# Performance work log

Measured on AMD Instinct MI355X. Metric: run time of the kernel, lower is better.

## Reference

```python
import jax, jax.numpy as jnp
import numpy as np

DIM = 1024
N_HEADS = 16
HEAD_DIM = DIM // N_HEADS
FF_DIM = 4096
EPS = 1e-8


def rms_norm(x, scale):
    # norm = ||x||_2 * d^{-1/2}; out = scale * x / (norm + eps)
    norm = jnp.linalg.norm(x, axis=-1, keepdims=True) * (x.shape[-1] ** -0.5)
    return scale * x / (norm + EPS)


def rope_cos_sin(seq_len, dtype=jnp.float32):
    # inv_freq over even indices of head_dim; after the truncation branch in
    # apply_rotary_pos_emb, effective cos/sin have size head_dim//2.
    inv_freq = 1.0 / (10000.0 ** (jnp.arange(0, HEAD_DIM, 2, dtype=jnp.float32) / HEAD_DIM))
    t = jnp.arange(seq_len, dtype=jnp.float32)
    freqs = t[:, None] * inv_freq[None, :]  # [S, head_dim//2]
    return jnp.cos(freqs).astype(dtype), jnp.sin(freqs).astype(dtype)


def apply_rope(x, cos, sin):
    # x: [B, S, H, hd]; cos/sin: [S, hd//2] broadcast over batch and heads
    c = cos[None, :, None, :]
    s = sin[None, :, None, :]
    x1, x2 = jnp.split(x, 2, axis=-1)
    return jnp.concatenate([x1 * c - x2 * s, x1 * s + x2 * c], axis=-1)


def setup_inputs() -> dict:
    key = jax.random.key(0)
    ks = jax.random.split(key, 10)
    B, S = 2, 2048
    std = DIM ** -0.5
    inp = {
        "x": jax.random.normal(ks[0], (B, S, DIM), jnp.float32),
        "mask": jnp.tril(jnp.ones((S, S), dtype=bool)),
        "qkv_w": jax.random.normal(ks[1], (3 * DIM, DIM), jnp.float32) * std,
        "attn_out_w": jax.random.normal(ks[2], (DIM, DIM), jnp.float32) * std,
        "gate_w": jax.random.normal(ks[3], (FF_DIM, DIM), jnp.float32) * std,
        "gate_b": jnp.zeros((FF_DIM,), jnp.float32),
        "lin_w": jax.random.normal(ks[4], (FF_DIM, DIM), jnp.float32) * std,
        "lin_b": jnp.zeros((FF_DIM,), jnp.float32),
        "ff_out_w": jax.random.normal(ks[5], (DIM, FF_DIM), jnp.float32) * (FF_DIM ** -0.5),
        "norm1_scale": jnp.ones((DIM,), jnp.float32),
        "norm2_scale": jnp.ones((DIM,), jnp.float32),
    }
    return inp


def reference(x, mask, qkv_w, attn_out_w, gate_w, gate_b, lin_w, lin_b,
              ff_out_w, norm1_scale, norm2_scale):
    B, S, _ = x.shape
    residual = x
    qkv = (x @ qkv_w.T).reshape(B, S, 3, N_HEADS, HEAD_DIM)
    q, k, v = qkv[:, :, 0], qkv[:, :, 1], qkv[:, :, 2]  # [B,S,H,hd]
    cos, sin = rope_cos_sin(S, x.dtype)
    q = apply_rope(q, cos, sin)
    k = apply_rope(k, cos, sin)
    # naive full attention, materializing [B,H,S,S] as the source does
    scores = jnp.einsum('bqhd,bkhd->bhqk', q, k) / jnp.sqrt(jnp.asarray(HEAD_DIM, x.dtype))
    scores = jnp.where(mask[None, None, :, :], scores, jnp.asarray(-1e9, x.dtype))
    attn = jax.nn.softmax(scores, axis=-1)
    out = jnp.einsum('bhqk,bkhd->bqhd', attn, v).reshape(B, S, DIM)
    out = out @ attn_out_w.T
    x = rms_norm(residual + out, norm1_scale)
    residual = x
    ff = jax.nn.sigmoid(x @ gate_w.T + gate_b) * (x @ lin_w.T + lin_b)
    ff = ff @ ff_out_w.T
    x = rms_norm(residual + ff, norm2_scale)
    return x
```

## Files before the change

kernel.cpp:

```cpp
#include <hip/hip_runtime.h>
#include <hip/hip_bf16.h>
#include <math.h>

#define DIMSZ 1024
#define NHEAD 16
#define HDIM 64
#define FFDIM 4096
#define SEQ 2048
#define NBATCH 2

typedef unsigned short ushortt;
typedef __attribute__((ext_vector_type(8))) short frag8;
typedef __attribute__((ext_vector_type(4))) float f32x4;

__device__ __forceinline__ float u2f(ushortt u) {
  return __uint_as_float(((unsigned)u) << 16);
}
__device__ __forceinline__ ushortt f2bu(float f) {
  unsigned x = __float_as_uint(f);
  return (ushortt)((x + 0x7FFFu + ((x >> 16) & 1u)) >> 16);
}

__global__ __launch_bounds__(256) void cast_f2b(
    const float* __restrict__ src, ushortt* __restrict__ dst, int n) {
  int i = (blockIdx.x * 256 + threadIdx.x) * 4;
  if (i >= n) return;
  float4 f = *(const float4*)(src + i);
  ushort4 u;
  u.x = f2bu(f.x); u.y = f2bu(f.y); u.z = f2bu(f.z); u.w = f2bu(f.w);
  *(ushort4*)(dst + i) = u;
}

__global__ __launch_bounds__(256) void cast_ff_chunk(
    const float* __restrict__ gate_w, const float* __restrict__ lin_w,
    const float* __restrict__ ffout_w, int c,
    ushortt* __restrict__ gcb, ushortt* __restrict__ lcb,
    ushortt* __restrict__ focb) {
  const int M1 = 1048576;
  int t = (blockIdx.x * 256 + threadIdx.x) * 4;
  const float* src;
  ushortt* dst;
  int e;
  if (t < M1) {
    e = t; src = gate_w + (size_t)c * M1 + e; dst = gcb + e;
  } else if (t < 2 * M1) {
    e = t - M1; src = lin_w + (size_t)c * M1 + e; dst = lcb + e;
  } else {
    e = t - 2 * M1;
    int n = e >> 10, k = e & 1023;
    src = ffout_w + (size_t)n * FFDIM + c * 1024 + k; dst = focb + e;
  }
  float4 f = *(const float4*)src;
  ushort4 u;
  u.x = f2bu(f.x); u.y = f2bu(f.y); u.z = f2bu(f.z); u.w = f2bu(f.w);
  *(ushort4*)dst = u;
}

template <int EPI>
__global__ __launch_bounds__(256) void gemm_mfma(
    const ushortt* __restrict__ A, const ushortt* __restrict__ W,
    void* __restrict__ Cv, const float* __restrict__ bias,
    const ushortt* __restrict__ other, int M, int N, int K, int first) {
  __shared__ __align__(16) short As[2][128 * 32];
  __shared__ __align__(16) short Bs[2][128 * 32];
  const int tid = threadIdx.x;
  const int wave = tid >> 6;
  const int lane = tid & 63;
  const int bm = blockIdx.y * 128;
  const int bn = blockIdx.x * 128;
  const int wm = (wave >> 1) * 64;
  const int wn = (wave & 1) * 64;

  f32x4 acc[4][4] = {};

  const int sr = lane >> 2;
  const int sc = (lane & 3) * 8;
  const ushortt* pa0 = A + (size_t)(bm + wave * 16 + sr) * K + sc;
  const ushortt* pa1 = pa0 + (size_t)64 * K;
  const ushortt* pb0 = W + (size_t)(bn + wave * 16 + sr) * K + sc;
  const ushortt* pb1 = pb0 + (size_t)64 * K;
  const int lo0 = (wave * 16) * 32;
  const int lo1 = (64 + wave * 16) * 32;

  const int fr = lane & 15;
  const int fq = (lane >> 4) * 8;
  const int nt = K >> 5;

  auto stage = [&](int t, int buf) {
    const int ko = t * 32;
    short* ab = &As[0][0] + buf * 4096;
    short* bb = &Bs[0][0] + buf * 4096;
    __builtin_amdgcn_global_load_lds(
        (const __attribute__((address_space(1))) void*)(pa0 + ko),
        (__attribute__((address_space(3))) void*)(ab + lo0), 16, 0, 0);
    __builtin_amdgcn_global_load_lds(
        (const __attribute__((address_space(1))) void*)(pa1 + ko),
        (__attribute__((address_space(3))) void*)(ab + lo1), 16, 0, 0);
    __builtin_amdgcn_global_load_lds(
        (const __attribute__((address_space(1))) void*)(pb0 + ko),
        (__attribute__((address_space(3))) void*)(bb + lo0), 16, 0, 0);
    __builtin_amdgcn_global_load_lds(
        (const __attribute__((address_space(1))) void*)(pb1 + ko),
        (__attribute__((address_space(3))) void*)(bb + lo1), 16, 0, 0);
  };

  stage(0, 0);
  __syncthreads();

  for (int t = 0; t < nt; ++t) {
    if (t + 1 < nt) stage(t + 1, (t + 1) & 1);
    const short* as = &As[0][0] + (t & 1) * 4096;
    const short* bs = &Bs[0][0] + (t & 1) * 4096;

    frag8 af[4], bf[4];
#pragma unroll
    for (int mi = 0; mi < 4; ++mi)
      af[mi] = *(const frag8*)&as[(wm + mi * 16 + fr) * 32 + fq];
#pragma unroll
    for (int ni = 0; ni < 4; ++ni)
      bf[ni] = *(const frag8*)&bs[(wn + ni * 16 + fr) * 32 + fq];
#pragma unroll
    for (int mi = 0; mi < 4; ++mi)
#pragma unroll
      for (int ni = 0; ni < 4; ++ni)
        acc[mi][ni] = __builtin_amdgcn_mfma_f32_16x16x32_bf16(
            af[mi], bf[ni], acc[mi][ni], 0, 0, 0);
    __syncthreads();
  }

  const int er = (lane >> 4) * 4;
  const int ec = lane & 15;
#pragma unroll
  for (int mi = 0; mi < 4; ++mi)
#pragma unroll
    for (int ni = 0; ni < 4; ++ni)
#pragma unroll
      for (int r = 0; r < 4; ++r) {
        int m = bm + wm + mi * 16 + er + r;
        int n = bn + wn + ni * 16 + ec;
        size_t o = (size_t)m * N + n;
        float v = acc[mi][ni][r];
        if (EPI == 0) {
          ((float*)Cv)[o] = v;
        } else if (EPI == 1) {
          ((ushortt*)Cv)[o] = f2bu(v);
        } else {
          float* C = (float*)Cv;
          C[o] = first ? v : C[o] + v;
        }
      }
}

__global__ __launch_bounds__(256) void gemm_gatelin(
    const ushortt* __restrict__ A, const ushortt* __restrict__ Wg,
    const ushortt* __restrict__ Wl, ushortt* __restrict__ Cv,
    const float* __restrict__ gbias, const float* __restrict__ lbias,
    int M, int N, int K) {
  __shared__ __align__(16) short As[2][128 * 32];
  __shared__ __align__(16) short Gs[2][128 * 32];
  __shared__ __align__(16) short Ls[2][128 * 32];
  const int tid = threadIdx.x;
  const int wave = tid >> 6;
  const int lane = tid & 63;
  const int bm = blockIdx.y * 128;
  const int bn = blockIdx.x * 128;
  const int wm = (wave >> 1) * 64;
  const int wn = (wave & 1) * 64;

  f32x4 accg[4][4] = {};
  f32x4 accl[4][4] = {};

  const int sr = lane >> 2;
  const int sc = (lane & 3) * 8;
  const ushortt* pa0 = A + (size_t)(bm + wave * 16 + sr) * K + sc;
  const ushortt* pa1 = pa0 + (size_t)64 * K;
  const ushortt* pg0 = Wg + (size_t)(bn + wave * 16 + sr) * K + sc;
  const ushortt* pg1 = pg0 + (size_t)64 * K;
  const ushortt* pl0 = Wl + (size_t)(bn + wave * 16 + sr) * K + sc;
  const ushortt* pl1 = pl0 + (size_t)64 * K;
  const int lo0 = (wave * 16) * 32;
  const int lo1 = (64 + wave * 16) * 32;

  const int fr = lane & 15;
  const int fq = (lane >> 4) * 8;
  const int nt = K >> 5;

  auto stage = [&](int t, int buf) {
    const int ko = t * 32;
    short* ab = &As[0][0] + buf * 4096;
    short* gb = &Gs[0][0] + buf * 4096;
    short* lb = &Ls[0][0] + buf * 4096;
    __builtin_amdgcn_global_load_lds(
        (const __attribute__((address_space(1))) void*)(pa0 + ko),
        (__attribute__((address_space(3))) void*)(ab + lo0), 16, 0, 0);
    __builtin_amdgcn_global_load_lds(
        (const __attribute__((address_space(1))) void*)(pa1 + ko),
        (__attribute__((address_space(3))) void*)(ab + lo1), 16, 0, 0);
    __builtin_amdgcn_global_load_lds(
        (const __attribute__((address_space(1))) void*)(pg0 + ko),
        (__attribute__((address_space(3))) void*)(gb + lo0), 16, 0, 0);
    __builtin_amdgcn_global_load_lds(
        (const __attribute__((address_space(1))) void*)(pg1 + ko),
        (__attribute__((address_space(3))) void*)(gb + lo1), 16, 0, 0);
    __builtin_amdgcn_global_load_lds(
        (const __attribute__((address_space(1))) void*)(pl0 + ko),
        (__attribute__((address_space(3))) void*)(lb + lo0), 16, 0, 0);
    __builtin_amdgcn_global_load_lds(
        (const __attribute__((address_space(1))) void*)(pl1 + ko),
        (__attribute__((address_space(3))) void*)(lb + lo1), 16, 0, 0);
  };

  stage(0, 0);
  __syncthreads();

  for (int t = 0; t < nt; ++t) {
    if (t + 1 < nt) stage(t + 1, (t + 1) & 1);
    const short* as = &As[0][0] + (t & 1) * 4096;
    const short* gs = &Gs[0][0] + (t & 1) * 4096;
    const short* ls = &Ls[0][0] + (t & 1) * 4096;

    frag8 af[4], gf[4], lf[4];
#pragma unroll
    for (int mi = 0; mi < 4; ++mi)
      af[mi] = *(const frag8*)&as[(wm + mi * 16 + fr) * 32 + fq];
#pragma unroll
    for (int ni = 0; ni < 4; ++ni) {
      gf[ni] = *(const frag8*)&gs[(wn + ni * 16 + fr) * 32 + fq];
      lf[ni] = *(const frag8*)&ls[(wn + ni * 16 + fr) * 32 + fq];
    }
#pragma unroll
    for (int mi = 0; mi < 4; ++mi)
#pragma unroll
      for (int ni = 0; ni < 4; ++ni) {
        accg[mi][ni] = __builtin_amdgcn_mfma_f32_16x16x32_bf16(
            af[mi], gf[ni], accg[mi][ni], 0, 0, 0);
        accl[mi][ni] = __builtin_amdgcn_mfma_f32_16x16x32_bf16(
            af[mi], lf[ni], accl[mi][ni], 0, 0, 0);
      }
    __syncthreads();
  }

  const int er = (lane >> 4) * 4;
  const int ec = lane & 15;
#pragma unroll
  for (int mi = 0; mi < 4; ++mi)
#pragma unroll
    for (int ni = 0; ni < 4; ++ni)
#pragma unroll
      for (int r = 0; r < 4; ++r) {
        int m = bm + wm + mi * 16 + er + r;
        int n = bn + wn + ni * 16 + ec;
        size_t o = (size_t)m * N + n;
        float g = accg[mi][ni][r] + gbias[n];
        float l = accl[mi][ni][r] + lbias[n];
        float sig = 1.0f / (1.0f + __expf(-g));
        ((ushortt*)Cv)[o] = f2bu(sig * l);
      }
}

__global__ __launch_bounds__(256) void rope_prep(
    const ushortt* __restrict__ qkv, ushortt* __restrict__ Qr,
    ushortt* __restrict__ Kr, ushortt* __restrict__ Vr) {
  const int s0 = blockIdx.x * 64;
  const int bh = blockIdx.y;
  const int b = bh >> 4, h = bh & 15;
  const int tid = threadIdx.x;
  __shared__ float ifr_s[32];
  __shared__ ushortt vt[64][72];
  if (tid < 32) ifr_s[tid] = __powf(10000.0f, -(float)tid * (1.0f / 32.0f));
  __syncthreads();
  const size_t qbase = (size_t)bh * SEQ * 64;

#pragma unroll
  for (int i = 0; i < 8; ++i) {
    int p = i * 256 + tid;
    int r = p >> 5, d = p & 31;
    size_t src = ((size_t)(b * SEQ + s0 + r)) * (3 * DIMSZ) + h * 64 + d;
    float q1 = u2f(qkv[src]), q2 = u2f(qkv[src + 32]);
    float k1 = u2f(qkv[src + DIMSZ]), k2 = u2f(qkv[src + DIMSZ + 32]);
    float ang = (float)(s0 + r) * ifr_s[d];
    float sn, cs;
    __sincosf(ang, &sn, &cs);
    size_t dst = qbase + (size_t)(s0 + r) * 64 + d;
    Qr[dst]      = f2bu((q1 * cs - q2 * sn) * 0.125f);
    Qr[dst + 32] = f2bu((q1 * sn + q2 * cs) * 0.125f);
    Kr[dst]      = f2bu(k1 * cs - k2 * sn);
    Kr[dst + 32] = f2bu(k1 * sn + k2 * cs);
  }

#pragma unroll
  for (int i = 0; i < 2; ++i) {
    int e = (i * 256 + tid) * 8;
    int r = e >> 6, d0 = e & 63;
    size_t src = ((size_t)(b * SEQ + s0 + r)) * (3 * DIMSZ) + 2 * DIMSZ + h * 64 + d0;
    *(ushort4*)&vt[r][d0]     = *(const ushort4*)(qkv + src);
    *(ushort4*)&vt[r][d0 + 4] = *(const ushort4*)(qkv + src + 4);
  }
  __syncthreads();
  {
    int d = tid >> 2;
    int sc0 = (tid & 3) * 16;
    size_t dst = (size_t)bh * 64 * SEQ + (size_t)blockIdx.x * 4096 +
                 (size_t)d * 64 + sc0;
    ushortt tmp[16];
#pragma unroll
    for (int j = 0; j < 16; ++j) tmp[j] = vt[sc0 + j][d];
    *(ushort4*)(Vr + dst)      = *(ushort4*)&tmp[0];
    *(ushort4*)(Vr + dst + 4)  = *(ushort4*)&tmp[4];
    *(ushort4*)(Vr + dst + 8)  = *(ushort4*)&tmp[8];
    *(ushort4*)(Vr + dst + 12) = *(ushort4*)&tmp[12];
  }
}

__global__ __launch_bounds__(512) void flash_mfma(
    const ushortt* __restrict__ Qr, const ushortt* __restrict__ Kr,
    const ushortt* __restrict__ Vr, ushortt* __restrict__ ctx) {
  const int id = blockIdx.x;
  const int qt = id >> 5;
  const int bh = id & 31;
  const int q0 = qt * 128;
  const int b = bh >> 4, h = bh & 15;
  const int tid = threadIdx.x;
  const int w = tid >> 6;
  const int lane = tid & 63;
  const int fr = lane & 15;
  const int quad = lane >> 4;

  __shared__ __align__(16) short Kb[2][4096];
  __shared__ __align__(16) short Vb[2][4096];
  __shared__ __align__(16) ushortt Ps[8][16][72];

  const size_t qkbase = (size_t)bh * SEQ * 64;
  const size_t vbase = (size_t)bh * 64 * SEQ;

  const int lin = (w << 10) + ((lane & 63) << 4);
  const int swz = lin ^ (((lin >> 7) & 7) << 4);
  const char* ksrc = (const char*)(Kr + qkbase) + swz;
  const char* vsrc = (const char*)(Vr + vbase) + swz;
  short* kdst[2] = {&Kb[0][w * 512], &Kb[1][w * 512]};
  short* vdst[2] = {&Vb[0][w * 512], &Vb[1][w * 512]};

  frag8 aq[2];
#pragma unroll
  for (int hh = 0; hh < 2; ++hh)
    aq[hh] = *(const frag8*)(Qr + qkbase + (size_t)(q0 + w * 16 + fr) * 64 +
                             hh * 32 + quad * 8);

  float mr[4], lr[4];
  f32x4 od[4] = {};
#pragma unroll
  for (int r = 0; r < 4; ++r) { mr[r] = -1e30f; lr[r] = 0.0f; }

  const int nt = 2 * qt + 2;

  __builtin_amdgcn_global_load_lds(
      (const __attribute__((address_space(1))) void*)ksrc,
      (__attribute__((address_space(3))) void*)kdst[0], 16, 0, 0);
  __builtin_amdgcn_global_load_lds(
      (const __attribute__((address_space(1))) void*)vsrc,
      (__attribute__((address_space(3))) void*)vdst[0], 16, 0, 0);
  __syncthreads();

  for (int t = 0; t < nt; ++t) {
    const int c0 = t * 64;
    if (t + 1 < nt) {
      const char* kn = ksrc + (size_t)(t + 1) * 8192;
      const char* vn = vsrc + (size_t)(t + 1) * 8192;
      __builtin_amdgcn_global_load_lds(
          (const __attribute__((address_space(1))) void*)kn,
          (__attribute__((address_space(3))) void*)kdst[(t + 1) & 1], 16, 0, 0);
      __builtin_amdgcn_global_load_lds(
          (const __attribute__((address_space(1))) void*)vn,
          (__attribute__((address_space(3))) void*)vdst[(t + 1) & 1], 16, 0, 0);
    }
    const char* kcur = (const char*)Kb[t & 1];
    const char* vcur = (const char*)Vb[t & 1];

    if (c0 <= q0 + w * 16 + 15) {
      f32x4 sc[4] = {};
#pragma unroll
      for (int ni = 0; ni < 4; ++ni)
#pragma unroll
        for (int hh = 0; hh < 2; ++hh) {
          int kb = (((ni * 16 + fr) << 7) + (hh << 6) + (quad << 4)) ^
                   ((fr & 7) << 4);
          frag8 kf = *(const frag8*)(kcur + kb);
          sc[ni] = __builtin_amdgcn_mfma_f32_16x16x32_bf16(aq[hh], kf, sc[ni],
                                                           0, 0, 0);
        }

      if (c0 + 63 > q0 + w * 16) {
        int rowb = q0 + w * 16 + quad * 4;
#pragma unroll
        for (int ni = 0; ni < 4; ++ni) {
          int col = c0 + ni * 16 + fr;
#pragma unroll
          for (int r = 0; r < 4; ++r)
            if (col > rowb + r) sc[ni][r] = -1e30f;
        }
      }

#pragma unroll
      for (int r = 0; r < 4; ++r) {
        float cm = fmaxf(fmaxf(sc[0][r], sc[1][r]), fmaxf(sc[2][r], sc[3][r]));
        for (int off = 1; off < 16; off <<= 1)
          cm = fmaxf(cm, __shfl_xor(cm, off, 16));
        float mn = fmaxf(mr[r], cm);
        float corr = __expf(mr[r] - mn);
        mr[r] = mn;
        float ps = 0.0f;
#pragma unroll
        for (int ni = 0; ni < 4; ++ni) {
          float p = __expf(sc[ni][r] - mn);
          Ps[w][quad * 4 + r][ni * 16 + fr] = f2bu(p);
          ps += p;
        }
        for (int off = 1; off < 16; off <<= 1) ps += __shfl_xor(ps, off, 16);
        lr[r] = lr[r] * corr + ps;
#pragma unroll
        for (int dt = 0; dt < 4; ++dt) od[dt][r] *= corr;
      }

      frag8 pf[2];
#pragma unroll
      for (int hh = 0; hh < 2; ++hh)
        pf[hh] = *(const frag8*)&Ps[w][fr][hh * 32 + quad * 8];
#pragma unroll
      for (int dt = 0; dt < 4; ++dt)
#pragma unroll
        for (int hh = 0; hh < 2; ++hh) {
          int vb_ = (((dt * 16 + fr) << 7) + (hh << 6) + (quad << 4)) ^
                    ((fr & 7) << 4);
          frag8 vf = *(const frag8*)(vcur + vb_);
          od[dt] = __builtin_amdgcn_mfma_f32_16x16x32_bf16(pf[hh], vf, od[dt],
                                                           0, 0, 0);
        }
    }
    __syncthreads();
  }

#pragma unroll
  for (int r = 0; r < 4; ++r) {
    float inv = 1.0f / lr[r];
    size_t row = (size_t)(b * SEQ + q0 + w * 16 + quad * 4 + r) * DIMSZ + h * 64;
#pragma unroll
    for (int dt = 0; dt < 4; ++dt)
      ctx[row + dt * 16 + fr] = f2bu(od[dt][r] * inv);
  }
}

template <int DUAL>
__global__ __launch_bounds__(256) void add_rmsnorm(
    const float* __restrict__ res, const float* __restrict__ proj,
    const float* __restrict__ scale, float* __restrict__ out,
    ushortt* __restrict__ out2) {
  const int row = blockIdx.x;
  const int tid = threadIdx.x;
  const size_t base = (size_t)row * DIMSZ;
  __shared__ float red[4];
  float y[4];
  float ss = 0.0f;
#pragma unroll
  for (int j = 0; j < 4; ++j) {
    int d = tid + j * 256;
    float yv = res[base + d] + proj[base + d];
    y[j] = yv;
    ss += yv * yv;
  }
  for (int off = 1; off < 64; off <<= 1) ss += __shfl_xor(ss, off, 64);
  if ((tid & 63) == 0) red[tid >> 6] = ss;
  __syncthreads();
  float tot = red[0] + red[1] + red[2] + red[3];
  float norm = sqrtf(tot) * 0.03125f;
  float inv = 1.0f / (norm + 1e-8f);
#pragma unroll
  for (int j = 0; j < 4; ++j) {
    int d = tid + j * 256;
    float v = scale[d] * y[j] * inv;
    out[base + d] = v;
    if (DUAL) out2[base + d] = f2bu(v);
  }
}

extern "C" void kernel_launch(void* const* d_in, const int* in_sizes, int n_in,
                              void* d_out, int out_size, void* d_ws, size_t ws_size,
                              hipStream_t stream) {
  const float* x          = (const float*)d_in[0];
  const float* qkv_w      = (const float*)d_in[2];
  const float* attn_out_w = (const float*)d_in[3];
  const float* gate_w     = (const float*)d_in[4];
  const float* gate_b     = (const float*)d_in[5];
  const float* lin_w      = (const float*)d_in[6];
  const float* lin_b      = (const float*)d_in[7];
  const float* ff_out_w   = (const float*)d_in[8];
  const float* n1s        = (const float*)d_in[9];
  const float* n2s        = (const float*)d_in[10];
  float* out = (float*)d_out;

  const int M = NBATCH * SEQ;
  char* ws = (char*)d_ws;
  char* dob = (char*)d_out;
  const size_t MB = 1 << 20;
  ushortt* qkv_tmp = (ushortt*)(ws + 0);
  ushortt* xb      = (ushortt*)(ws + 24 * MB);
  ushortt* qkv_wb  = (ushortt*)(ws + 32 * MB);
  ushortt* Qr      = (ushortt*)(ws + 24 * MB);
  ushortt* Kr      = (ushortt*)(ws + 32 * MB);
  ushortt* Vr      = (ushortt*)(ws + 40 * MB);
  ushortt* attn_wb = (ushortt*)(ws + 24 * MB);
  float*   proj    = (float*)(ws + 0);
  float*   x1      = (float*)(ws + 16 * MB);
  ushortt* x1b     = (ushortt*)(ws + 32 * MB);
  float*   proj2   = (float*)(ws + 0);
  ushortt* gcb     = (ushortt*)(ws + 40 * MB);
  ushortt* lcb     = (ushortt*)(ws + 42 * MB);
  ushortt* focb    = (ushortt*)(ws + 44 * MB);
  ushortt* ctx  = (ushortt*)(dob + 0);
  ushortt* ffc  = (ushortt*)(dob + 0);

  cast_f2b<<<4194304 / 1024, 256, 0, stream>>>(x, xb, 4194304);
  cast_f2b<<<3145728 / 1024, 256, 0, stream>>>(qkv_w, qkv_wb, 3145728);
  gemm_mfma<1><<<dim3(3072 / 128, M / 128), 256, 0, stream>>>(
      xb, qkv_wb, qkv_tmp, nullptr, nullptr, M, 3072, DIMSZ, 0);
  rope_prep<<<dim3(SEQ / 64, NBATCH * NHEAD), 256, 0, stream>>>(
      qkv_tmp, Qr, Kr, Vr);
  flash_mfma<<<(SEQ / 128) * NBATCH * NHEAD, 512, 0, stream>>>(
      Qr, Kr, Vr, ctx);
  cast_f2b<<<1048576 / 1024, 256, 0, stream>>>(attn_out_w, attn_wb, 1048576);
  gemm_mfma<0><<<dim3(DIMSZ / 128, M / 128), 256, 0, stream>>>(
      ctx, attn_wb, proj, nullptr, nullptr, M, DIMSZ, DIMSZ, 0);
  add_rmsnorm<1><<<M, 256, 0, stream>>>(x, proj, n1s, x1, x1b);
  for (int c = 0; c < 4; ++c) {
    cast_ff_chunk<<<3072, 256, 0, stream>>>(gate_w, lin_w, ff_out_w, c,
                                            gcb, lcb, focb);
    gemm_gatelin<<<dim3(1024 / 128, M / 128), 256, 0, stream>>>(
        x1b, gcb, lcb, ffc, gate_b + c * 1024, lin_b + c * 1024,
        M, 1024, DIMSZ);
    gemm_mfma<4><<<dim3(DIMSZ / 128, M / 128), 256, 0, stream>>>(
        ffc, focb, proj2, nullptr, nullptr, M, DIMSZ, 1024, c == 0 ? 1 : 0);
  }
  add_rmsnorm<0><<<M, 256, 0, stream>>>(x1, proj2, n2s, out, nullptr);
}
```

Measured before the change: 615.1 us.

## Fuse ff_out weight cast into GEMM, halve FF chunks, balance causal attention order

Adds a gemm_ffout kernel that loads fp32 ff_out weights directly, converts them to bf16 in registers and stages them through LDS, which removes the separate cast of that weight. The FF loop now runs 2 chunks of 2048 instead of 4 chunks of 1024, giving fewer launches and fewer read-modify-write passes over proj2. Flash attention block ids are remapped so the second half of the grid visits query tiles in reverse order, to balance the uneven causal work across the grid. The risk is extra per-thread conversion work and register pressure inside the ff_out GEMM mainloop.

```diff
diff --git a/kernel.cpp b/kernel.cpp
--- a/kernel.cpp
+++ b/kernel.cpp
@@ -31,36 +31,10 @@
   *(ushort4*)(dst + i) = u;
 }
 
-__global__ __launch_bounds__(256) void cast_ff_chunk(
-    const float* __restrict__ gate_w, const float* __restrict__ lin_w,
-    const float* __restrict__ ffout_w, int c,
-    ushortt* __restrict__ gcb, ushortt* __restrict__ lcb,
-    ushortt* __restrict__ focb) {
-  const int M1 = 1048576;
-  int t = (blockIdx.x * 256 + threadIdx.x) * 4;
-  const float* src;
-  ushortt* dst;
-  int e;
-  if (t < M1) {
-    e = t; src = gate_w + (size_t)c * M1 + e; dst = gcb + e;
-  } else if (t < 2 * M1) {
-    e = t - M1; src = lin_w + (size_t)c * M1 + e; dst = lcb + e;
-  } else {
-    e = t - 2 * M1;
-    int n = e >> 10, k = e & 1023;
-    src = ffout_w + (size_t)n * FFDIM + c * 1024 + k; dst = focb + e;
-  }
-  float4 f = *(const float4*)src;
-  ushort4 u;
-  u.x = f2bu(f.x); u.y = f2bu(f.y); u.z = f2bu(f.z); u.w = f2bu(f.w);
-  *(ushort4*)dst = u;
-}
-
 template <int EPI>
 __global__ __launch_bounds__(256) void gemm_mfma(
     const ushortt* __restrict__ A, const ushortt* __restrict__ W,
-    void* __restrict__ Cv, const float* __restrict__ bias,
-    const ushortt* __restrict__ other, int M, int N, int K, int first) {
+    void* __restrict__ Cv, int M, int N, int K) {
   __shared__ __align__(16) short As[2][128 * 32];
   __shared__ __align__(16) short Bs[2][128 * 32];
   const int tid = threadIdx.x;
@@ -142,11 +116,8 @@
         float v = acc[mi][ni][r];
         if (EPI == 0) {
           ((float*)Cv)[o] = v;
-        } else if (EPI == 1) {
+        } else {
           ((ushortt*)Cv)[o] = f2bu(v);
-        } else {
-          float* C = (float*)Cv;
-          C[o] = first ? v : C[o] + v;
         }
       }
 }
@@ -258,6 +229,113 @@
       }
 }
 
+__global__ __launch_bounds__(256) void gemm_ffout(
+    const ushortt* __restrict__ A, const float* __restrict__ Bw,
+    float* __restrict__ C, int lda, int koff, int first) {
+  __shared__ __align__(16) short As[2][128 * 32];
+  __shared__ __align__(16) short Bs[2][128 * 32];
+  const int tid = threadIdx.x;
+  const int wave = tid >> 6;
+  const int lane = tid & 63;
+  const int bm = blockIdx.y * 128;
+  const int bn = blockIdx.x * 128;
+  const int wm = (wave >> 1) * 64;
+  const int wn = (wave & 1) * 64;
+
+  f32x4 acc[4][4] = {};
+
+  const int sr = lane >> 2;
+  const int sc = (lane & 3) * 8;
+  const ushortt* pa0 = A + (size_t)(bm + wave * 16 + sr) * lda + sc;
+  const ushortt* pa1 = pa0 + (size_t)64 * lda;
+  const int lo0 = (wave * 16) * 32;
+  const int lo1 = (64 + wave * 16) * 32;
+
+  const int br = tid >> 2;
+  const int kc = (tid & 3) * 8;
+  const float* pb0 = Bw + (size_t)(bn + br) * FFDIM + koff + kc;
+  const float* pb1 = pb0 + (size_t)64 * FFDIM;
+
+  const int fr = lane & 15;
+  const int fq = (lane >> 4) * 8;
+  const int nt = 2048 >> 5;
+
+  float4 f0, f1, f2, f3;
+  auto bload = [&](int t) {
+    const float* p0 = pb0 + t * 32;
+    const float* p1 = pb1 + t * 32;
+    f0 = *(const float4*)p0; f1 = *(const float4*)(p0 + 4);
+    f2 = *(const float4*)p1; f3 = *(const float4*)(p1 + 4);
+  };
+  auto pk = [&](float4 a, float4 b) {
+    frag8 v;
+    v[0] = (short)f2bu(a.x); v[1] = (short)f2bu(a.y);
+    v[2] = (short)f2bu(a.z); v[3] = (short)f2bu(a.w);
+    v[4] = (short)f2bu(b.x); v[5] = (short)f2bu(b.y);
+    v[6] = (short)f2bu(b.z); v[7] = (short)f2bu(b.w);
+    return v;
+  };
+  auto bwrite = [&](int buf) {
+    *(frag8*)&Bs[buf][tid * 8] = pk(f0, f1);
+    *(frag8*)&Bs[buf][2048 + tid * 8] = pk(f2, f3);
+  };
+  auto astage = [&](int t, int buf) {
+    const int ko = t * 32;
+    short* ab = &As[0][0] + buf * 4096;
+    __builtin_amdgcn_global_load_lds(
+        (const __attribute__((address_space(1))) void*)(pa0 + ko),
+        (__attribute__((address_space(3))) void*)(ab + lo0), 16, 0, 0);
+    __builtin_amdgcn_global_load_lds(
+        (const __attribute__((address_space(1))) void*)(pa1 + ko),
+        (__attribute__((address_space(3))) void*)(ab + lo1), 16, 0, 0);
+  };
+
+  astage(0, 0);
+  bload(0);
+  bwrite(0);
+  __syncthreads();
+
+  for (int t = 0; t < nt; ++t) {
+    if (t + 1 < nt) {
+      astage(t + 1, (t + 1) & 1);
+      bload(t + 1);
+    }
+    const short* as = &As[0][0] + (t & 1) * 4096;
+    const short* bs = &Bs[0][0] + (t & 1) * 4096;
+
+    frag8 af[4], bf[4];
+#pragma unroll
+    for (int mi = 0; mi < 4; ++mi)
+      af[mi] = *(const frag8*)&as[(wm + mi * 16 + fr) * 32 + fq];
+#pragma unroll
+    for (int ni = 0; ni < 4; ++ni)
+      bf[ni] = *(const frag8*)&bs[(wn + ni * 16 + fr) * 32 + fq];
+#pragma unroll
+    for (int mi = 0; mi < 4; ++mi)
+#pragma unroll
+      for (int ni = 0; ni < 4; ++ni)
+        acc[mi][ni] = __builtin_amdgcn_mfma_f32_16x16x32_bf16(
+            af[mi], bf[ni], acc[mi][ni], 0, 0, 0);
+    if (t + 1 < nt) bwrite((t + 1) & 1);
+    __syncthreads();
+  }
+
+  const int er = (lane >> 4) * 4;
+  const int ec = lane & 15;
+#pragma unroll
+  for (int mi = 0; mi < 4; ++mi)
+#pragma unroll
+    for (int ni = 0; ni < 4; ++ni)
+#pragma unroll
+      for (int r = 0; r < 4; ++r) {
+        int m = bm + wm + mi * 16 + er + r;
+        int n = bn + wn + ni * 16 + ec;
+        size_t o = (size_t)m * 1024 + n;
+        float v = acc[mi][ni][r];
+        C[o] = first ? v : C[o] + v;
+      }
+}
+
 __global__ __launch_bounds__(256) void rope_prep(
     const ushortt* __restrict__ qkv, ushortt* __restrict__ Qr,
     ushortt* __restrict__ Kr, ushortt* __restrict__ Vr) {
@@ -316,8 +394,10 @@
     const ushortt* __restrict__ Qr, const ushortt* __restrict__ Kr,
     const ushortt* __restrict__ Vr, ushortt* __restrict__ ctx) {
   const int id = blockIdx.x;
-  const int qt = id >> 5;
-  const int bh = id & 31;
+  const int r5 = id & 255;
+  const int qt0 = r5 >> 5;
+  const int qt = (id & 256) ? (15 - qt0) : qt0;
+  const int bh = r5 & 31;
   const int q0 = qt * 128;
   const int b = bh >> 4, h = bh & 15;
   const int tid = threadIdx.x;
@@ -513,31 +593,32 @@
   ushortt* x1b     = (ushortt*)(ws + 32 * MB);
   float*   proj2   = (float*)(ws + 0);
   ushortt* gcb     = (ushortt*)(ws + 40 * MB);
-  ushortt* lcb     = (ushortt*)(ws + 42 * MB);
-  ushortt* focb    = (ushortt*)(ws + 44 * MB);
+  ushortt* lcb     = (ushortt*)(ws + 44 * MB);
   ushortt* ctx  = (ushortt*)(dob + 0);
   ushortt* ffc  = (ushortt*)(dob + 0);
 
   cast_f2b<<<4194304 / 1024, 256, 0, stream>>>(x, xb, 4194304);
   cast_f2b<<<3145728 / 1024, 256, 0, stream>>>(qkv_w, qkv_wb, 3145728);
   gemm_mfma<1><<<dim3(3072 / 128, M / 128), 256, 0, stream>>>(
-      xb, qkv_wb, qkv_tmp, nullptr, nullptr, M, 3072, DIMSZ, 0);
+      xb, qkv_wb, qkv_tmp, M, 3072, DIMSZ);
   rope_prep<<<dim3(SEQ / 64, NBATCH * NHEAD), 256, 0, stream>>>(
       qkv_tmp, Qr, Kr, Vr);
   flash_mfma<<<(SEQ / 128) * NBATCH * NHEAD, 512, 0, stream>>>(
       Qr, Kr, Vr, ctx);
   cast_f2b<<<1048576 / 1024, 256, 0, stream>>>(attn_out_w, attn_wb, 1048576);
   gemm_mfma<0><<<dim3(DIMSZ / 128, M / 128), 256, 0, stream>>>(
-      ctx, attn_wb, proj, nullptr, nullptr, M, DIMSZ, DIMSZ, 0);
+      ctx, attn_wb, proj, M, DIMSZ, DIMSZ);
   add_rmsnorm<1><<<M, 256, 0, stream>>>(x, proj, n1s, x1, x1b);
-  for (int c = 0; c < 4; ++c) {
-    cast_ff_chunk<<<3072, 256, 0, stream>>>(gate_w, lin_w, ff_out_w, c,
-                                            gcb, lcb, focb);
-    gemm_gatelin<<<dim3(1024 / 128, M / 128), 256, 0, stream>>>(
-        x1b, gcb, lcb, ffc, gate_b + c * 1024, lin_b + c * 1024,
-        M, 1024, DIMSZ);
-    gemm_mfma<4><<<dim3(DIMSZ / 128, M / 128), 256, 0, stream>>>(
-        ffc, focb, proj2, nullptr, nullptr, M, DIMSZ, 1024, c == 0 ? 1 : 0);
+  for (int c = 0; c < 2; ++c) {
+    cast_f2b<<<2048, 256, 0, stream>>>(
+        gate_w + (size_t)c * 2097152, gcb, 2097152);
+    cast_f2b<<<2048, 256, 0, stream>>>(
+        lin_w + (size_t)c * 2097152, lcb, 2097152);
+    gemm_gatelin<<<dim3(2048 / 128, M / 128), 256, 0, stream>>>(
+        x1b, gcb, lcb, ffc, gate_b + c * 2048, lin_b + c * 2048,
+        M, 2048, DIMSZ);
+    gemm_ffout<<<dim3(1024 / 128, M / 128), 256, 0, stream>>>(
+        ffc, ff_out_w, proj2, 2048, c * 2048, c == 0 ? 1 : 0);
   }
   add_rmsnorm<0><<<M, 256, 0, stream>>>(x1, proj2, n2s, out, nullptr);
 }
```

After: 607.5 us. Within noise of the previous version (-1.2%).
